# Performance work log

Measured on AMD Instinct MI355X. Metric: run time of the kernel, lower is better.

Reference implementation:

```python
import jax, jax.numpy as jnp
import numpy as np

N_HEADS = 32
N_KV_HEADS = 8
ROPE_BASE = 500000.0


def setup_inputs() -> dict:
    key = jax.random.key(0)
    k1, k2, k3 = jax.random.split(key, 3)
    B, S, D = 2, 2048, 4096
    head_dim = D // N_HEADS
    qkv_out = (N_HEADS + 2 * N_KV_HEADS) * head_dim  # 6144
    x = jax.random.normal(k1, (B, S, D), dtype=jnp.float32)
    Wqkv = jax.random.normal(k2, (qkv_out, D), dtype=jnp.float32) * (1.0 / np.sqrt(D))
    Wo = jax.random.normal(k3, (D, D), dtype=jnp.float32) * (1.0 / np.sqrt(D))
    return {"x": x, "Wqkv": Wqkv, "Wo": Wo}


def _rope_tables(seq_len, head_dim, dtype):
    # inv_freq over even indices of head_dim (half-split RoPE)
    inv_freq = 1.0 / (ROPE_BASE ** (jnp.arange(0, head_dim, 2, dtype=jnp.float32) / head_dim))
    t = jnp.arange(seq_len, dtype=jnp.float32)
    freqs = jnp.outer(t, inv_freq)  # [S, head_dim//2]
    return jnp.cos(freqs).astype(dtype), jnp.sin(freqs).astype(dtype)


def _apply_rope(x, cos, sin):
    # x: [B, H, S, hd]; cos/sin: [S, hd//2] -> broadcast [1,1,S,hd//2]
    hd = x.shape[-1]
    x1, x2 = x[..., : hd // 2], x[..., hd // 2 :]
    c = cos[None, None]
    s = sin[None, None]
    return jnp.concatenate([x1 * c - x2 * s, x2 * c + x1 * s], axis=-1)


def reference(x, Wqkv, Wo):
    B, S, D = x.shape
    head_dim = D // N_HEADS
    n_rep = N_HEADS // N_KV_HEADS
    q_size = N_HEADS * head_dim
    kv_size = N_KV_HEADS * head_dim

    qkv = jnp.einsum("bsd,od->bso", x, Wqkv)  # fused QKV projection
    q = qkv[..., :q_size].reshape(B, S, N_HEADS, head_dim).transpose(0, 2, 1, 3)
    k = qkv[..., q_size : q_size + kv_size].reshape(B, S, N_KV_HEADS, head_dim).transpose(0, 2, 1, 3)
    v = qkv[..., q_size + kv_size :].reshape(B, S, N_KV_HEADS, head_dim).transpose(0, 2, 1, 3)

    cos, sin = _rope_tables(S, head_dim, x.dtype)
    q = _apply_rope(q, cos, sin)
    k = _apply_rope(k, cos, sin)

    # GQA expansion: repeat each kv head n_rep times (matches repeat_interleave indices)
    k = jnp.repeat(k, n_rep, axis=1)  # [B, H, S, hd]
    v = jnp.repeat(v, n_rep, axis=1)

    scale = 1.0 / jnp.sqrt(jnp.asarray(head_dim, dtype=x.dtype))
    scores = jnp.einsum("bhqd,bhkd->bhqk", q, k) * scale
    causal = jnp.tril(jnp.ones((S, S), dtype=bool))
    scores = jnp.where(causal[None, None], scores, jnp.finfo(scores.dtype).min)
    attn = jax.nn.softmax(scores, axis=-1)
    out = jnp.einsum("bhqk,bhkd->bhqd", attn, v)
    out = out.transpose(0, 2, 1, 3).reshape(B, S, D)
    return jnp.einsum("bsd,od->bso", out, Wo)
```

## Files before the change

### kernel.cpp

```cpp
#include <hip/hip_runtime.h>
#include <stdint.h>

#define BB 2
#define SS 2048
#define DD 4096
#define NH 32
#define NKVH 8
#define HD 128
#define QKVN 6144
#define MROWS (BB * SS)
#define LOG2E 1.4426950408889634f

typedef short bf16x8 __attribute__((ext_vector_type(8)));
typedef float f32x4 __attribute__((ext_vector_type(4)));

__device__ __forceinline__ short f32_bf16(float f) {
  union { float f; unsigned u; } c; c.f = f;
  unsigned r = (c.u + 0x7fffu + ((c.u >> 16) & 1u)) >> 16;
  return (short)r;
}
__device__ __forceinline__ float bf16_f32(short h) {
  union { unsigned u; float f; } c; c.u = ((unsigned)(unsigned short)h) << 16;
  return c.f;
}

__device__ __forceinline__ void async16(const void* g, void* l) {
  __builtin_amdgcn_global_load_lds(
      (const __attribute__((address_space(1))) unsigned int*)(uintptr_t)g,
      (__attribute__((address_space(3))) unsigned int*)(uintptr_t)l,
      16, 0, 0);
}

__global__ __launch_bounds__(256) void cast_bf16_kernel(const float* __restrict__ in,
                                                        short* __restrict__ out, int n4) {
  int i = blockIdx.x * 256 + threadIdx.x;
  if (i >= n4) return;
  float4 v = ((const float4*)in)[i];
  short4 o;
  o.x = f32_bf16(v.x); o.y = f32_bf16(v.y); o.z = f32_bf16(v.z); o.w = f32_bf16(v.w);
  ((short4*)out)[i] = o;
}

__global__ __launch_bounds__(256) void rope_tables_kernel(float* __restrict__ cosT,
                                                          float* __restrict__ sinT) {
  int idx = blockIdx.x * 256 + threadIdx.x;
  if (idx >= SS * 64) return;
  int s = idx >> 6, t = idx & 63;
  float invf = exp2f(-(float)t * (18.931568569324174f / 64.0f));
  float fr = (float)s * invf;
  float sv, cv;
  sincosf(fr, &sv, &cv);
  cosT[idx] = cv;
  sinT[idx] = sv;
}

__global__ __launch_bounds__(256) void rope_scatter_kernel(const short* __restrict__ qkv,
    const float* __restrict__ cosT, const float* __restrict__ sinT,
    short* __restrict__ Qb, short* __restrict__ Kb) {
  int idx = blockIdx.x * 256 + threadIdx.x;
  if (idx >= BB * SS * 40 * 64) return;
  int t = idx & 63;
  int hh = (idx >> 6) % 40;
  int bs = (idx >> 6) / 40;
  int s = bs & (SS - 1);
  int b = bs >> 11;
  const short* row = qkv + (long)bs * QKVN + hh * HD;
  float x1 = bf16_f32(row[t]);
  float x2 = bf16_f32(row[t + 64]);
  float c = cosT[(s << 6) + t], sn = sinT[(s << 6) + t];
  float o1 = x1 * c - x2 * sn;
  float o2 = x2 * c + x1 * sn;
  if (hh < 32) {
    const float sc = 0.08838834764831845f;
    o1 *= sc; o2 *= sc;
    short* q = Qb + ((long)(b * NH + hh) * SS + s) * HD;
    q[t] = f32_bf16(o1); q[t + 64] = f32_bf16(o2);
  } else {
    short* k = Kb + ((long)(b * NKVH + (hh - 32)) * SS + s) * HD;
    k[t] = f32_bf16(o1); k[t + 64] = f32_bf16(o2);
  }
}

__global__ __launch_bounds__(256) void v_scatter_kernel(const short* __restrict__ qkv,
                                                        short* __restrict__ Vtb) {
  int bid = blockIdx.x;
  int s0 = (bid & 31) << 6;
  int kvh = (bid >> 5) & 7;
  int b = bid >> 8;
  const short* src = qkv + (long)(b * SS + s0) * QKVN + 5120 + kvh * HD;
  short* dst = Vtb + ((long)(b * NKVH + kvh) * HD) * SS + s0;
  int w = threadIdx.x >> 6, l = threadIdx.x & 63;
#pragma unroll
  for (int it = 0; it < 32; ++it) {
    int d = (it << 2) + w;
    dst[(long)d * SS + l] = src[(long)l * QKVN + d];
  }
}

#define STAGE256(kt, bsel)                                                          \
  {                                                                                 \
    const long kbase_ = (long)(kt) << 6;                                            \
    _Pragma("unroll") for (int i_ = 0; i_ < 4; i_++) {                              \
      const int idx_ = tid + i_ * 512;                                              \
      const int row_ = idx_ >> 3, slot_ = idx_ & 7;                                 \
      const int ss_ = slot_ ^ (row_ & 7);                                           \
      async16(Ag0 + (long)row_ * K + kbase_ + ss_ * 8,                              \
              &Abuf[bsel][row_ * 64 + slot_ * 8]);                                  \
      async16(Bg0 + (long)row_ * K + kbase_ + ss_ * 8,                              \
              &Bbuf[bsel][row_ * 64 + slot_ * 8]);                                  \
    }                                                                               \
  }

#define GPHASE(p, LASTP)                                                            \
  {                                                                                 \
    bf16x8 afr[2][2];                                                               \
    _Pragma("unroll") for (int mi = 0; mi < 2; mi++)                                \
      _Pragma("unroll") for (int kk = 0; kk < 2; kk++)                              \
        afr[mi][kk] = *(const bf16x8*)&Ac[(((p) * 2 + mi) * 16 + l16) * 64 +        \
                                          ((((kk << 2) + quad) ^ xr) << 3)];        \
    __builtin_amdgcn_s_barrier();                                                   \
    asm volatile("s_waitcnt lgkmcnt(0)" ::: "memory");                              \
    __builtin_amdgcn_sched_barrier(0);                                              \
    __builtin_amdgcn_s_setprio(1);                                                  \
    _Pragma("unroll") for (int mi = 0; mi < 2; mi++)                                \
      _Pragma("unroll") for (int nr = 0; nr < 4; nr++)                              \
        _Pragma("unroll") for (int kk = 0; kk < 2; kk++)                            \
          acc[(p) * 2 + mi][nr] = __builtin_amdgcn_mfma_f32_16x16x32_bf16(          \
              afr[mi][kk], bfr[nr][kk], acc[(p) * 2 + mi][nr], 0, 0, 0);            \
    __builtin_amdgcn_s_setprio(0);                                                  \
    if (!(LASTP)) __builtin_amdgcn_s_barrier();                                     \
  }

template <int STORE_BF16>
__global__ __launch_bounds__(512) void gemm256_kernel(const short* __restrict__ A,
    const short* __restrict__ B, void* __restrict__ Cv, int M, int N, int K, int gx) {
  __shared__ __align__(16) short Abuf[2][256 * 64];
  __shared__ __align__(16) short Bbuf[2][256 * 64];
  const int tid = threadIdx.x;
  const int lane = tid & 63, wave = tid >> 6;
  const int quad = lane >> 4, l16 = lane & 15;
  const int wm = wave >> 2;
  const int wn = wave & 3;
  const int xr = l16 & 7;

  const int nwg = gridDim.x;
  const int cpx = nwg >> 3;
  const int wg = ((int)blockIdx.x & 7) * cpx + ((int)blockIdx.x >> 3);
  const int m0 = (wg / gx) << 8;
  const int n0 = (wg % gx) << 8;

  const short* Ag0 = A + (long)m0 * K;
  const short* Bg0 = B + (long)n0 * K;

  f32x4 acc[8][4];
#pragma unroll
  for (int mr = 0; mr < 8; mr++)
#pragma unroll
    for (int nr = 0; nr < 4; nr++) acc[mr][nr] = (f32x4){0.f, 0.f, 0.f, 0.f};

  const int nk = K >> 6;

  STAGE256(0, 0);
  asm volatile("s_waitcnt vmcnt(0)" ::: "memory");
  __builtin_amdgcn_sched_barrier(0);
  __builtin_amdgcn_s_barrier();

  int cur = 0;
#pragma unroll 1
  for (int kt = 0; kt < nk; ++kt) {
    if (kt + 1 < nk) {
      if (cur == 0) { STAGE256(kt + 1, 1); } else { STAGE256(kt + 1, 0); }
    }
    const short* Ac = &Abuf[cur][wm * 128 * 64];
    const short* Bc = &Bbuf[cur][wn * 64 * 64];

    bf16x8 bfr[4][2];
#pragma unroll
    for (int nr = 0; nr < 4; nr++)
#pragma unroll
      for (int kk = 0; kk < 2; kk++)
        bfr[nr][kk] = *(const bf16x8*)&Bc[(nr * 16 + l16) * 64 +
                                          ((((kk << 2) + quad) ^ xr) << 3)];
    GPHASE(0, 0)
    GPHASE(1, 0)
    GPHASE(2, 0)
    GPHASE(3, 1)

    asm volatile("s_waitcnt vmcnt(0)" ::: "memory");
    __builtin_amdgcn_sched_barrier(0);
    __builtin_amdgcn_s_barrier();
    cur ^= 1;
  }

#pragma unroll
  for (int mr = 0; mr < 8; mr++)
#pragma unroll
    for (int nr = 0; nr < 4; nr++)
#pragma unroll
      for (int r = 0; r < 4; r++) {
        long row = m0 + wm * 128 + mr * 16 + quad * 4 + r;
        long col = n0 + wn * 64 + nr * 16 + l16;
        if (STORE_BF16)
          ((short*)Cv)[row * N + col] = f32_bf16(acc[mr][nr][r]);
        else
          ((float*)Cv)[row * N + col] = acc[mr][nr][r];
      }
}

#define PSS 72

__global__ __launch_bounds__(256, 2) void flash_attn_kernel(const short* __restrict__ Q,
    const short* __restrict__ Kt, const short* __restrict__ Vt, short* __restrict__ O) {
  __shared__ __align__(16) short Ps[4][32 * PSS];
  const int tid = threadIdx.x;
  const int wave = tid >> 6, lane = tid & 63;
  const int quad = lane >> 4, l16 = lane & 15;

  const int flat = blockIdx.x;
  const int xcd = flat & 7;
  const int kk_ = flat >> 3;
  const int gsel = kk_ >> 5;
  const int jj = kk_ & 31;
  const int g = xcd * 2 + gsel;
  const int b = g >> 3, kvh = g & 7;
  const int h = (kvh << 2) + (jj >> 3);
  const int qb0 = jj & 7;

  const short* Kb = Kt + (long)(b * NKVH + kvh) * SS * HD;
  const short* Vb = Vt + (long)(b * NKVH + kvh) * HD * SS;
  short* Pw = &Ps[wave][0];

#pragma unroll 1
  for (int half = 0; half < 2; half++) {
    const int qb = half ? (15 - qb0) : qb0;
    const int w = half ? (3 - wave) : wave;
    const int q0w = (qb << 7) + (w << 5);

    const short* Qw = Q + ((long)(b * NH + h) * SS + q0w) * HD;
    bf16x8 qf[2][4];
#pragma unroll
    for (int i = 0; i < 2; i++)
#pragma unroll
      for (int kk = 0; kk < 4; kk++)
        qf[i][kk] = *(const bf16x8*)&Qw[(i * 16 + l16) * HD + kk * 32 + quad * 8];

    f32x4 oacc[2][8];
#pragma unroll
    for (int i = 0; i < 2; i++)
#pragma unroll
      for (int jo = 0; jo < 8; jo++) oacc[i][jo] = (f32x4){0.f, 0.f, 0.f, 0.f};
    float l_i[2][4];
#pragma unroll
    for (int i = 0; i < 2; i++)
#pragma unroll
      for (int r = 0; r < 4; r++) l_i[i][r] = 0.f;

    const int nfull = q0w >> 6;

#pragma unroll 1
    for (int t = 0; t <= nfull; t++) {
      const int j0 = t << 6;
      const bool last = (t == nfull);

      bf16x8 kf[16];
#pragma unroll
      for (int kk = 0; kk < 4; kk++)
#pragma unroll
        for (int j = 0; j < 4; j++)
          kf[kk * 4 + j] =
              *(const bf16x8*)&Kb[(long)(j0 + j * 16 + l16) * HD + kk * 32 + quad * 8];

      f32x4 sc[2][4];
#pragma unroll
      for (int i = 0; i < 2; i++)
#pragma unroll
        for (int j = 0; j < 4; j++) sc[i][j] = (f32x4){0.f, 0.f, 0.f, 0.f};
      __builtin_amdgcn_s_setprio(1);
#pragma unroll
      for (int kk = 0; kk < 4; kk++)
#pragma unroll
        for (int i = 0; i < 2; i++)
#pragma unroll
          for (int j = 0; j < 4; j++)
            sc[i][j] = __builtin_amdgcn_mfma_f32_16x16x32_bf16(qf[i][kk], kf[kk * 4 + j],
                                                               sc[i][j], 0, 0, 0);
      __builtin_amdgcn_s_setprio(0);

      bf16x8 vfa[8];
#pragma unroll
      for (int jo = 0; jo < 8; jo++)
        vfa[jo] = *(const bf16x8*)&Vb[(long)(jo * 16 + l16) * SS + j0 + quad * 8];

      if (last) {
#pragma unroll
        for (int i = 0; i < 2; i++)
#pragma unroll
          for (int r = 0; r < 4; r++) {
            int row = q0w + i * 16 + quad * 4 + r;
#pragma unroll
            for (int j = 0; j < 4; j++) {
              int col = j0 + j * 16 + l16;
              if (col > row) sc[i][j][r] = -3.0e38f;
            }
          }
      }

#pragma unroll
      for (int i = 0; i < 2; i++)
#pragma unroll
        for (int r = 0; r < 4; r++) {
          float ps = 0.f;
#pragma unroll
          for (int j = 0; j < 4; j++) {
            float p = __builtin_amdgcn_exp2f(sc[i][j][r] * LOG2E);
            sc[i][j][r] = p;
            ps += p;
          }
          l_i[i][r] += ps;
        }

#pragma unroll
      for (int i = 0; i < 2; i++)
#pragma unroll
        for (int j = 0; j < 4; j++)
#pragma unroll
          for (int r = 0; r < 4; r++)
            Pw[(i * 16 + quad * 4 + r) * PSS + j * 16 + l16] = f32_bf16(sc[i][j][r]);
      asm volatile("s_waitcnt lgkmcnt(0)" ::: "memory");

      bf16x8 ap[2][2];
#pragma unroll
      for (int kv = 0; kv < 2; kv++) {
        ap[kv][0] = *(const bf16x8*)&Pw[l16 * PSS + kv * 32 + quad * 8];
        ap[kv][1] = *(const bf16x8*)&Pw[(16 + l16) * PSS + kv * 32 + quad * 8];
      }

      bf16x8 vfb[8];
#pragma unroll
      for (int jo = 0; jo < 8; jo++)
        vfb[jo] = *(const bf16x8*)&Vb[(long)(jo * 16 + l16) * SS + j0 + 32 + quad * 8];

      __builtin_amdgcn_s_setprio(1);
#pragma unroll
      for (int jo = 0; jo < 8; jo++) {
        oacc[0][jo] = __builtin_amdgcn_mfma_f32_16x16x32_bf16(ap[0][0], vfa[jo],
                                                              oacc[0][jo], 0, 0, 0);
        oacc[1][jo] = __builtin_amdgcn_mfma_f32_16x16x32_bf16(ap[0][1], vfa[jo],
                                                              oacc[1][jo], 0, 0, 0);
      }
#pragma unroll
      for (int jo = 0; jo < 8; jo++) {
        oacc[0][jo] = __builtin_amdgcn_mfma_f32_16x16x32_bf16(ap[1][0], vfb[jo],
                                                              oacc[0][jo], 0, 0, 0);
        oacc[1][jo] = __builtin_amdgcn_mfma_f32_16x16x32_bf16(ap[1][1], vfb[jo],
                                                              oacc[1][jo], 0, 0, 0);
      }
      __builtin_amdgcn_s_setprio(0);
    }

    short* Ob = O + (long)(b * SS + q0w) * DD + h * HD;
#pragma unroll
    for (int i = 0; i < 2; i++)
#pragma unroll
      for (int r = 0; r < 4; r++) {
        float s = l_i[i][r];
        s += __shfl_xor(s, 1, 64);
        s += __shfl_xor(s, 2, 64);
        s += __shfl_xor(s, 4, 64);
        s += __shfl_xor(s, 8, 64);
        float inv = 1.0f / s;
        int row = i * 16 + quad * 4 + r;
#pragma unroll
        for (int jo = 0; jo < 8; jo++)
          Ob[(long)row * DD + jo * 16 + l16] = f32_bf16(oacc[i][jo][r] * inv);
      }
  }
}

extern "C" void kernel_launch(void* const* d_in, const int* in_sizes, int n_in,
                              void* d_out, int out_size, void* d_ws, size_t ws_size,
                              hipStream_t stream) {
  (void)in_sizes; (void)n_in; (void)out_size; (void)ws_size;
  const float* x    = (const float*)d_in[0];
  const float* Wqkv = (const float*)d_in[1];
  const float* Wo   = (const float*)d_in[2];
  char* ws = (char*)d_ws;
  short* xb    = (short*)(ws + 0);
  short* wqkvb = (short*)(ws + 33554432);
  short* qkvb  = (short*)(ws + 83886080);
  short* Qb    = (short*)(ws + 134217728);
  short* Kb    = (short*)(ws + 167772160);
  short* Vtb   = (short*)(ws + 176160768);
  float* cosT  = (float*)(ws + 184549376);
  float* sinT  = (float*)(ws + 185073664);
  short* wob   = qkvb;
  short* attnb = xb;

  cast_bf16_kernel<<<16384, 256, 0, stream>>>(x, xb, 4194304);
  cast_bf16_kernel<<<24576, 256, 0, stream>>>(Wqkv, wqkvb, 6291456);
  gemm256_kernel<1><<<dim3((QKVN / 256) * (MROWS / 256)), 512, 0, stream>>>(
      xb, wqkvb, (void*)qkvb, MROWS, QKVN, DD, QKVN / 256);
  rope_tables_kernel<<<512, 256, 0, stream>>>(cosT, sinT);
  rope_scatter_kernel<<<40960, 256, 0, stream>>>(qkvb, cosT, sinT, Qb, Kb);
  v_scatter_kernel<<<512, 256, 0, stream>>>(qkvb, Vtb);
  cast_bf16_kernel<<<16384, 256, 0, stream>>>(Wo, wob, 4194304);
  flash_attn_kernel<<<512, 256, 0, stream>>>(Qb, Kb, Vtb, attnb);
  gemm256_kernel<0><<<dim3((DD / 256) * (MROWS / 256)), 512, 0, stream>>>(
      attnb, wob, d_out, MROWS, DD, DD, DD / 256);
}
```

Measured before the change: 869.5 us.

## Stage K/V tiles in swizzled LDS via async copies shared across waves

Each wave previously loaded its own K and V fragments straight from global memory. Now the whole block cooperatively stages each 64-key K tile and V tile into XOR-swizzled shared memory with async copies, prefetching the next tile while the current one is consumed. Waves that have finished their causal range sit idle through the extra steps but still join the barriers. The goal is to cut redundant global/L2 traffic by a factor of four across waves, in exchange for several block barriers per tile, more LDS use and no more per-wave load balancing through the reversed wave order.

```diff
diff --git a/kernel.cpp b/kernel.cpp
--- a/kernel.cpp
+++ b/kernel.cpp
@@ -209,12 +209,35 @@
 
 #define PSS 72
 
+#define STAGEK(j0_)                                                                 \
+  {                                                                                 \
+    _Pragma("unroll") for (int i_ = 0; i_ < 4; i_++) {                              \
+      const int idx_ = tid + i_ * 256;                                              \
+      const int r_ = idx_ >> 4, s_ = idx_ & 15;                                     \
+      async16(Kb + (long)((j0_) + r_) * HD + ((s_ ^ (r_ & 7)) << 3),                \
+              &Ks[r_ * 128 + (s_ << 3)]);                                           \
+    }                                                                               \
+  }
+
+#define STAGEV(j0_)                                                                 \
+  {                                                                                 \
+    _Pragma("unroll") for (int i_ = 0; i_ < 4; i_++) {                              \
+      const int idx_ = tid + i_ * 256;                                              \
+      const int r_ = idx_ >> 3, s_ = idx_ & 7;                                      \
+      async16(Vb + (long)r_ * SS + (j0_) + ((s_ ^ (r_ & 7)) << 3),                  \
+              &Vs[r_ * 64 + (s_ << 3)]);                                            \
+    }                                                                               \
+  }
+
 __global__ __launch_bounds__(256, 2) void flash_attn_kernel(const short* __restrict__ Q,
     const short* __restrict__ Kt, const short* __restrict__ Vt, short* __restrict__ O) {
+  __shared__ __align__(16) short Ks[64 * 128];
+  __shared__ __align__(16) short Vs[128 * 64];
   __shared__ __align__(16) short Ps[4][32 * PSS];
   const int tid = threadIdx.x;
   const int wave = tid >> 6, lane = tid & 63;
   const int quad = lane >> 4, l16 = lane & 15;
+  const int k7 = l16 & 7;
 
   const int flat = blockIdx.x;
   const int xcd = flat & 7;
@@ -233,8 +256,10 @@
 #pragma unroll 1
   for (int half = 0; half < 2; half++) {
     const int qb = half ? (15 - qb0) : qb0;
-    const int w = half ? (3 - wave) : wave;
-    const int q0w = (qb << 7) + (w << 5);
+    const int q0b = qb << 7;
+    const int q0w = q0b + (wave << 5);
+    const int nfull = q0w >> 6;
+    const int tsteps = (q0b >> 6) + 2;
 
     const short* Qw = Q + ((long)(b * NH + h) * SS + q0w) * HD;
     bf16x8 qf[2][4];
@@ -243,6 +268,8 @@
 #pragma unroll
       for (int kk = 0; kk < 4; kk++)
         qf[i][kk] = *(const bf16x8*)&Qw[(i * 16 + l16) * HD + kk * 32 + quad * 8];
+    asm volatile("s_waitcnt vmcnt(0)" ::: "memory");
+    __builtin_amdgcn_sched_barrier(0);
 
     f32x4 oacc[2][8];
 #pragma unroll
@@ -255,107 +282,126 @@
 #pragma unroll
       for (int r = 0; r < 4; r++) l_i[i][r] = 0.f;
 
-    const int nfull = q0w >> 6;
+    STAGEK(0)
+    STAGEV(0)
 
 #pragma unroll 1
-    for (int t = 0; t <= nfull; t++) {
+    for (int t = 0; t < tsteps; t++) {
       const int j0 = t << 6;
-      const bool last = (t == nfull);
-
-      bf16x8 kf[16];
-#pragma unroll
-      for (int kk = 0; kk < 4; kk++)
-#pragma unroll
-        for (int j = 0; j < 4; j++)
-          kf[kk * 4 + j] =
-              *(const bf16x8*)&Kb[(long)(j0 + j * 16 + l16) * HD + kk * 32 + quad * 8];
+      const bool active = (t <= nfull);
+      const bool havenext = (t + 1 < tsteps);
+
+      asm volatile("s_waitcnt vmcnt(4)" ::: "memory");
+      __builtin_amdgcn_sched_barrier(0);
+      __builtin_amdgcn_s_barrier();
+      __builtin_amdgcn_sched_barrier(0);
 
       f32x4 sc[2][4];
-#pragma unroll
-      for (int i = 0; i < 2; i++)
-#pragma unroll
-        for (int j = 0; j < 4; j++) sc[i][j] = (f32x4){0.f, 0.f, 0.f, 0.f};
-      __builtin_amdgcn_s_setprio(1);
-#pragma unroll
-      for (int kk = 0; kk < 4; kk++)
+      if (active) {
+        bf16x8 kf[16];
+#pragma unroll
+        for (int kk = 0; kk < 4; kk++)
+#pragma unroll
+          for (int j = 0; j < 4; j++)
+            kf[kk * 4 + j] = *(const bf16x8*)&Ks[(j * 16 + l16) * 128 +
+                                                 ((((kk << 2) + quad) ^ k7) << 3)];
 #pragma unroll
         for (int i = 0; i < 2; i++)
 #pragma unroll
+          for (int j = 0; j < 4; j++) sc[i][j] = (f32x4){0.f, 0.f, 0.f, 0.f};
+        __builtin_amdgcn_s_setprio(1);
+#pragma unroll
+        for (int kk = 0; kk < 4; kk++)
+#pragma unroll
+          for (int i = 0; i < 2; i++)
+#pragma unroll
+            for (int j = 0; j < 4; j++)
+              sc[i][j] = __builtin_amdgcn_mfma_f32_16x16x32_bf16(
+                  qf[i][kk], kf[kk * 4 + j], sc[i][j], 0, 0, 0);
+        __builtin_amdgcn_s_setprio(0);
+      }
+
+      __builtin_amdgcn_s_barrier();
+      __builtin_amdgcn_sched_barrier(0);
+      if (havenext) STAGEK(j0 + 64)
+
+      if (active) {
+        if (t == nfull) {
+#pragma unroll
+          for (int i = 0; i < 2; i++)
+#pragma unroll
+            for (int r = 0; r < 4; r++) {
+              int row = q0w + i * 16 + quad * 4 + r;
+#pragma unroll
+              for (int j = 0; j < 4; j++) {
+                int col = j0 + j * 16 + l16;
+                if (col > row) sc[i][j][r] = -3.0e38f;
+              }
+            }
+        }
+#pragma unroll
+        for (int i = 0; i < 2; i++)
+#pragma unroll
+          for (int r = 0; r < 4; r++) {
+            float ps = 0.f;
+#pragma unroll
+            for (int j = 0; j < 4; j++) {
+              float p = __builtin_amdgcn_exp2f(sc[i][j][r] * LOG2E);
+              sc[i][j][r] = p;
+              ps += p;
+            }
+            l_i[i][r] += ps;
+          }
+#pragma unroll
+        for (int i = 0; i < 2; i++)
+#pragma unroll
           for (int j = 0; j < 4; j++)
-            sc[i][j] = __builtin_amdgcn_mfma_f32_16x16x32_bf16(qf[i][kk], kf[kk * 4 + j],
-                                                               sc[i][j], 0, 0, 0);
-      __builtin_amdgcn_s_setprio(0);
-
-      bf16x8 vfa[8];
-#pragma unroll
-      for (int jo = 0; jo < 8; jo++)
-        vfa[jo] = *(const bf16x8*)&Vb[(long)(jo * 16 + l16) * SS + j0 + quad * 8];
-
-      if (last) {
-#pragma unroll
-        for (int i = 0; i < 2; i++)
-#pragma unroll
-          for (int r = 0; r < 4; r++) {
-            int row = q0w + i * 16 + quad * 4 + r;
-#pragma unroll
-            for (int j = 0; j < 4; j++) {
-              int col = j0 + j * 16 + l16;
-              if (col > row) sc[i][j][r] = -3.0e38f;
-            }
-          }
-      }
-
-#pragma unroll
-      for (int i = 0; i < 2; i++)
-#pragma unroll
-        for (int r = 0; r < 4; r++) {
-          float ps = 0.f;
-#pragma unroll
-          for (int j = 0; j < 4; j++) {
-            float p = __builtin_amdgcn_exp2f(sc[i][j][r] * LOG2E);
-            sc[i][j][r] = p;
-            ps += p;
-          }
-          l_i[i][r] += ps;
+#pragma unroll
+            for (int r = 0; r < 4; r++)
+              Pw[(i * 16 + quad * 4 + r) * PSS + j * 16 + l16] = f32_bf16(sc[i][j][r]);
+      }
+
+      if (havenext) {
+        asm volatile("s_waitcnt vmcnt(4)" ::: "memory");
+      } else {
+        asm volatile("s_waitcnt vmcnt(0)" ::: "memory");
+      }
+      __builtin_amdgcn_sched_barrier(0);
+      __builtin_amdgcn_s_barrier();
+      __builtin_amdgcn_sched_barrier(0);
+
+      if (active) {
+        asm volatile("s_waitcnt lgkmcnt(0)" ::: "memory");
+        bf16x8 ap[2][2];
+#pragma unroll
+        for (int kv = 0; kv < 2; kv++) {
+          ap[kv][0] = *(const bf16x8*)&Pw[l16 * PSS + kv * 32 + quad * 8];
+          ap[kv][1] = *(const bf16x8*)&Pw[(16 + l16) * PSS + kv * 32 + quad * 8];
         }
-
-#pragma unroll
-      for (int i = 0; i < 2; i++)
-#pragma unroll
-        for (int j = 0; j < 4; j++)
-#pragma unroll
-          for (int r = 0; r < 4; r++)
-            Pw[(i * 16 + quad * 4 + r) * PSS + j * 16 + l16] = f32_bf16(sc[i][j][r]);
-      asm volatile("s_waitcnt lgkmcnt(0)" ::: "memory");
-
-      bf16x8 ap[2][2];
-#pragma unroll
-      for (int kv = 0; kv < 2; kv++) {
-        ap[kv][0] = *(const bf16x8*)&Pw[l16 * PSS + kv * 32 + quad * 8];
-        ap[kv][1] = *(const bf16x8*)&Pw[(16 + l16) * PSS + kv * 32 + quad * 8];
-      }
-
-      bf16x8 vfb[8];
-#pragma unroll
-      for (int jo = 0; jo < 8; jo++)
-        vfb[jo] = *(const bf16x8*)&Vb[(long)(jo * 16 + l16) * SS + j0 + 32 + quad * 8];
-
-      __builtin_amdgcn_s_setprio(1);
-#pragma unroll
-      for (int jo = 0; jo < 8; jo++) {
-        oacc[0][jo] = __builtin_amdgcn_mfma_f32_16x16x32_bf16(ap[0][0], vfa[jo],
-                                                              oacc[0][jo], 0, 0, 0);
-        oacc[1][jo] = __builtin_amdgcn_mfma_f32_16x16x32_bf16(ap[0][1], vfa[jo],
-                                                              oacc[1][jo], 0, 0, 0);
-      }
-#pragma unroll
-      for (int jo = 0; jo < 8; jo++) {
-        oacc[0][jo] = __builtin_amdgcn_mfma_f32_16x16x32_bf16(ap[1][0], vfb[jo],
-                                                              oacc[0][jo], 0, 0, 0);
-        oacc[1][jo] = __builtin_amdgcn_mfma_f32_16x16x32_bf16(ap[1][1], vfb[jo],
-                                                              oacc[1][jo], 0, 0, 0);
-      }
-      __builtin_amdgcn_s_setprio(0);
+        __builtin_amdgcn_s_setprio(1);
+#pragma unroll
+        for (int jo = 0; jo < 8; jo++) {
+          bf16x8 v0 = *(const bf16x8*)&Vs[(jo * 16 + l16) * 64 + ((quad ^ k7) << 3)];
+          oacc[0][jo] = __builtin_amdgcn_mfma_f32_16x16x32_bf16(ap[0][0], v0,
+                                                                oacc[0][jo], 0, 0, 0);
+          oacc[1][jo] = __builtin_amdgcn_mfma_f32_16x16x32_bf16(ap[0][1], v0,
+                                                                oacc[1][jo], 0, 0, 0);
+        }
+#pragma unroll
+        for (int jo = 0; jo < 8; jo++) {
+          bf16x8 v1 = *(const bf16x8*)&Vs[(jo * 16 + l16) * 64 +
+                                          (((4 + quad) ^ k7) << 3)];
+          oacc[0][jo] = __builtin_amdgcn_mfma_f32_16x16x32_bf16(ap[1][0], v1,
+                                                                oacc[0][jo], 0, 0, 0);
+          oacc[1][jo] = __builtin_amdgcn_mfma_f32_16x16x32_bf16(ap[1][1], v1,
+                                                                oacc[1][jo], 0, 0, 0);
+        }
+        __builtin_amdgcn_s_setprio(0);
+      }
+
+      __builtin_amdgcn_s_barrier();
+      __builtin_amdgcn_sched_barrier(0);
+      if (havenext) STAGEV(j0 + 64)
     }
 
     short* Ob = O + (long)(b * SS + q0w) * DD + h * HD;
```

Result: faster. 724.2 us (-16.7%).
